# Kernel tuning notes

Hardware: AMD Instinct MI355X
Metric: run time of the kernel (lower is better)

Reference implementation:

```python
import jax, jax.numpy as jnp
import numpy as np

N_NODES = 50000
N_EDGES = 800000
D_IN = 96
D_OUT = 96


def setup_inputs() -> dict:
    key = jax.random.key(0)
    k1, k2, k3, k4, k5 = jax.random.split(key, 5)
    x = jax.random.normal(k1, (N_NODES, D_IN), dtype=jnp.float32)
    edge_w = jax.random.uniform(k2, (N_EDGES,), dtype=jnp.float32)
    weight = jax.random.normal(k3, (D_IN, D_OUT), dtype=jnp.float32) * (1.0 / np.sqrt(D_IN))
    bias = jnp.zeros((D_OUT,), dtype=jnp.float32)
    row = jax.random.randint(k4, (N_EDGES,), 0, N_NODES, dtype=jnp.int32)
    col = jax.random.randint(k5, (N_EDGES,), 0, N_NODES, dtype=jnp.int32)
    return {"x": x, "edge_w": edge_w, "weight": weight, "bias": bias, "row": row, "col": col}


def reference(x, edge_w, weight, bias, row, col):
    # hidden_hat = support @ x, with support given in COO form (row, col, edge_w)
    # gather source-node features, scale by edge weight, scatter-add to destination
    msgs = edge_w[:, None] * x[col]                      # [E, D_in]
    hidden_hat = jax.ops.segment_sum(msgs, row, num_segments=N_NODES)  # [N, D_in]
    # hidden_tilde = hidden_hat @ W + b
    hidden_tilde = jnp.dot(hidden_hat, weight) + bias    # [N, D_out]
    return jax.nn.relu(hidden_tilde)
```

## Files before the change

kernel.cpp:

```cpp
#include <hip/hip_runtime.h>
#include <hip/hip_fp16.h>

#define N_NODES 50000
#define N_EDGES 800000
#define D 96
#define D4 (D / 4)

#define BIN_SH 6
#define BIN_NODES 64
#define NBINS 782
#define MAXB 1536

#define TBLOCKS 782
#define SBLOCKS 196
#define EPB 4082
#define WT_LD 104

typedef _Float16 f16x8 __attribute__((ext_vector_type(8)));
typedef float    f32x4 __attribute__((ext_vector_type(4)));

__global__ __launch_bounds__(256) void transform_scatter(
        const float* __restrict__ x, const float* __restrict__ W,
        const int* __restrict__ row, const int* __restrict__ col,
        const float* __restrict__ edge_w,
        __half* __restrict__ y, int* __restrict__ cursor,
        int2* __restrict__ binned) {
    __shared__ __align__(16) int smem[5000];
    const int t = threadIdx.x;
    const int bid = blockIdx.x;

    if (bid >= TBLOCKS) {
        int* lh    = smem;
        int* gbase = smem + NBINS;
        int* lcur  = smem + 2 * NBINS;
        for (int i = t; i < NBINS; i += 256) { lh[i] = 0; lcur[i] = 0; }
        __syncthreads();
        int e0 = (bid - TBLOCKS) * EPB;
        int e1 = min(e0 + EPB, N_EDGES);
        for (int e = e0 + t; e < e1; e += 256)
            atomicAdd(&lh[row[e] >> BIN_SH], 1);
        __syncthreads();
        for (int i = t; i < NBINS; i += 256)
            gbase[i] = lh[i] ? (i * MAXB + atomicAdd(&cursor[i], lh[i])) : 0;
        __syncthreads();
        for (int e = e0 + t; e < e1; e += 256) {
            int r = row[e];
            int b = r >> BIN_SH;
            int p = atomicAdd(&lcur[b], 1);
            binned[gbase[b] + p] = make_int2(col[e] | ((r & 63) << 16),
                                             __float_as_int(edge_w[e]));
        }
        return;
    }

    _Float16* WT = reinterpret_cast<_Float16*>(smem);
    for (int i = t; i < D * D; i += 256) {
        int k = i / D, n2 = i % D;
        WT[n2 * WT_LD + k] = (_Float16)W[i];
    }
    __syncthreads();

    const int lane = t & 63;
    const int wv   = t >> 6;
    const int wid  = bid * 4 + wv;
    const int n0   = wid * 16;
    if (n0 >= N_NODES) return;

    const int arow = lane & 15;
    const int kgrp = lane >> 4;

    const float4* xr = reinterpret_cast<const float4*>(x) +
                       (long long)(n0 + arow) * D4;
    f16x8 afrag[3];
    #pragma unroll
    for (int ks = 0; ks < 3; ++ks) {
        float4 v0 = xr[ks * 8 + kgrp * 2];
        float4 v1 = xr[ks * 8 + kgrp * 2 + 1];
        f16x8 a;
        a[0] = (_Float16)v0.x; a[1] = (_Float16)v0.y;
        a[2] = (_Float16)v0.z; a[3] = (_Float16)v0.w;
        a[4] = (_Float16)v1.x; a[5] = (_Float16)v1.y;
        a[6] = (_Float16)v1.z; a[7] = (_Float16)v1.w;
        afrag[ks] = a;
    }

    const int bcol = lane & 15;
    #pragma unroll
    for (int nt = 0; nt < 6; ++nt) {
        f32x4 acc = {0.f, 0.f, 0.f, 0.f};
        #pragma unroll
        for (int ks = 0; ks < 3; ++ks) {
            f16x8 b = *reinterpret_cast<const f16x8*>(
                &WT[(nt * 16 + bcol) * WT_LD + ks * 32 + kgrp * 8]);
            acc = __builtin_amdgcn_mfma_f32_16x16x32_f16(afrag[ks], b, acc, 0, 0, 0);
        }
        #pragma unroll
        for (int i = 0; i < 4; ++i) {
            int rrow = kgrp * 4 + i;
            y[(long long)(n0 + rrow) * D + nt * 16 + bcol] = __float2half_rn(acc[i]);
        }
    }
}

__global__ __launch_bounds__(768) void binsort_aggregate(
        const int* __restrict__ cursor, const int2* __restrict__ binned,
        const __half* __restrict__ y, const float* __restrict__ bias,
        float* __restrict__ out) {
    __shared__ int2 recs[MAXB];
    __shared__ int hist[BIN_NODES];
    __shared__ int sc[BIN_NODES];
    __shared__ int lcur[BIN_NODES];
    __shared__ int nodeoff[BIN_NODES + 1];
    int t = threadIdx.x;
    int b = blockIdx.x;
    int base = b * MAXB;
    int size = cursor[b];
    if (size > MAXB) size = MAXB;
    if (t < BIN_NODES) hist[t] = 0;
    __syncthreads();

    int2 rl0, rl1;
    int i0 = t, i1 = t + 768;
    if (i0 < size) { rl0 = binned[base + i0]; atomicAdd(&hist[(rl0.x >> 16) & 63], 1); }
    if (i1 < size) { rl1 = binned[base + i1]; atomicAdd(&hist[(rl1.x >> 16) & 63], 1); }
    __syncthreads();

    int h = 0;
    if (t < BIN_NODES) { h = hist[t]; sc[t] = h; }
    for (int off = 1; off < BIN_NODES; off <<= 1) {
        __syncthreads();
        int a = (t >= off && t < BIN_NODES) ? sc[t - off] : 0;
        __syncthreads();
        if (t < BIN_NODES) sc[t] += a;
    }
    __syncthreads();
    if (t < BIN_NODES) { int excl = sc[t] - h; nodeoff[t] = excl; lcur[t] = excl; }
    if (t == 0) nodeoff[BIN_NODES] = size;
    __syncthreads();

    if (i0 < size) { int lr = (rl0.x >> 16) & 63; int p = atomicAdd(&lcur[lr], 1);
                     recs[p] = make_int2(rl0.x & 0xFFFF, rl0.y); }
    if (i1 < size) { int lr = (rl1.x >> 16) & 63; int p = atomicAdd(&lcur[lr], 1);
                     recs[p] = make_int2(rl1.x & 0xFFFF, rl1.y); }
    __syncthreads();

    const uint4* yu = reinterpret_cast<const uint4*>(y);
    int c = t % 12;
    int g = t / 12;
    int n = (b << BIN_SH) + g;
    if (n >= N_NODES) return;
    int beg = nodeoff[g];
    int end = nodeoff[g + 1];

    float acc[8], acc2[8];
    #pragma unroll
    for (int i = 0; i < 8; ++i) { acc[i] = 0.0f; acc2[i] = 0.0f; }

    int j = beg;
    for (; j + 1 < end; j += 2) {
        int2 r0 = recs[j];
        int2 r1 = recs[j + 1];
        float w0 = __int_as_float(r0.y);
        float w1 = __int_as_float(r1.y);
        uint4 v0 = yu[(long long)r0.x * 12 + c];
        uint4 v1 = yu[(long long)r1.x * 12 + c];
        float2 a0 = __half22float2(*reinterpret_cast<const __half2*>(&v0.x));
        float2 a1 = __half22float2(*reinterpret_cast<const __half2*>(&v0.y));
        float2 a2 = __half22float2(*reinterpret_cast<const __half2*>(&v0.z));
        float2 a3 = __half22float2(*reinterpret_cast<const __half2*>(&v0.w));
        acc[0] = fmaf(w0, a0.x, acc[0]);
        acc[1] = fmaf(w0, a0.y, acc[1]);
        acc[2] = fmaf(w0, a1.x, acc[2]);
        acc[3] = fmaf(w0, a1.y, acc[3]);
        acc[4] = fmaf(w0, a2.x, acc[4]);
        acc[5] = fmaf(w0, a2.y, acc[5]);
        acc[6] = fmaf(w0, a3.x, acc[6]);
        acc[7] = fmaf(w0, a3.y, acc[7]);
        float2 b0 = __half22float2(*reinterpret_cast<const __half2*>(&v1.x));
        float2 b1 = __half22float2(*reinterpret_cast<const __half2*>(&v1.y));
        float2 b2 = __half22float2(*reinterpret_cast<const __half2*>(&v1.z));
        float2 b3 = __half22float2(*reinterpret_cast<const __half2*>(&v1.w));
        acc2[0] = fmaf(w1, b0.x, acc2[0]);
        acc2[1] = fmaf(w1, b0.y, acc2[1]);
        acc2[2] = fmaf(w1, b1.x, acc2[2]);
        acc2[3] = fmaf(w1, b1.y, acc2[3]);
        acc2[4] = fmaf(w1, b2.x, acc2[4]);
        acc2[5] = fmaf(w1, b2.y, acc2[5]);
        acc2[6] = fmaf(w1, b3.x, acc2[6]);
        acc2[7] = fmaf(w1, b3.y, acc2[7]);
    }
    if (j < end) {
        int2 r0 = recs[j];
        float w0 = __int_as_float(r0.y);
        uint4 v0 = yu[(long long)r0.x * 12 + c];
        float2 a0 = __half22float2(*reinterpret_cast<const __half2*>(&v0.x));
        float2 a1 = __half22float2(*reinterpret_cast<const __half2*>(&v0.y));
        float2 a2 = __half22float2(*reinterpret_cast<const __half2*>(&v0.z));
        float2 a3 = __half22float2(*reinterpret_cast<const __half2*>(&v0.w));
        acc[0] = fmaf(w0, a0.x, acc[0]);
        acc[1] = fmaf(w0, a0.y, acc[1]);
        acc[2] = fmaf(w0, a1.x, acc[2]);
        acc[3] = fmaf(w0, a1.y, acc[3]);
        acc[4] = fmaf(w0, a2.x, acc[4]);
        acc[5] = fmaf(w0, a2.y, acc[5]);
        acc[6] = fmaf(w0, a3.x, acc[6]);
        acc[7] = fmaf(w0, a3.y, acc[7]);
    }
    #pragma unroll
    for (int i = 0; i < 8; ++i) acc[i] += acc2[i];

    const float4* b4 = reinterpret_cast<const float4*>(bias);
    float4 ba = b4[c * 2], bb = b4[c * 2 + 1];
    float4 o0, o1;
    o0.x = fmaxf(acc[0] + ba.x, 0.f);
    o0.y = fmaxf(acc[1] + ba.y, 0.f);
    o0.z = fmaxf(acc[2] + ba.z, 0.f);
    o0.w = fmaxf(acc[3] + ba.w, 0.f);
    o1.x = fmaxf(acc[4] + bb.x, 0.f);
    o1.y = fmaxf(acc[5] + bb.y, 0.f);
    o1.z = fmaxf(acc[6] + bb.z, 0.f);
    o1.w = fmaxf(acc[7] + bb.w, 0.f);
    float4* op = reinterpret_cast<float4*>(&out[(long long)n * D + c * 8]);
    op[0] = o0;
    op[1] = o1;
}

__global__ void zero_f32(float* __restrict__ p, long long n) {
    long long i = (long long)blockIdx.x * blockDim.x + threadIdx.x;
    long long stride = (long long)gridDim.x * blockDim.x;
    for (; i < n; i += stride) p[i] = 0.0f;
}

__global__ __launch_bounds__(256) void scatter_edges(
        const float* __restrict__ x, const float* __restrict__ edge_w,
        const int* __restrict__ row, const int* __restrict__ col,
        float* __restrict__ hidden) {
    long long t = (long long)blockIdx.x * blockDim.x + threadIdx.x;
    const long long total = (long long)N_EDGES * D4;
    if (t >= total) return;
    int e = (int)(t / D4);
    int c = (int)(t % D4);
    float w = edge_w[e];
    const float4 v = *reinterpret_cast<const float4*>(&x[(long long)col[e] * D + c * 4]);
    float* o = &hidden[(long long)row[e] * D + c * 4];
    atomicAdd(o + 0, w * v.x);
    atomicAdd(o + 1, w * v.y);
    atomicAdd(o + 2, w * v.z);
    atomicAdd(o + 3, w * v.w);
}

__global__ __launch_bounds__(256) void gemm_bias_relu(
        const float* __restrict__ hidden, const float* __restrict__ W,
        const float* __restrict__ bias, float* __restrict__ out) {
    __shared__ float Ws[D * D];
    __shared__ float bs[D];
    for (int i = threadIdx.x; i < D * D; i += blockDim.x) Ws[i] = W[i];
    if (threadIdx.x < D) bs[threadIdx.x] = bias[threadIdx.x];
    __syncthreads();
    const long long total = (long long)N_NODES * D;
    long long stride = (long long)gridDim.x * blockDim.x;
    for (long long idx = (long long)blockIdx.x * blockDim.x + threadIdx.x;
         idx < total; idx += stride) {
        int n = (int)(idx / D);
        int d = (int)(idx % D);
        const float* hrow = &hidden[(long long)n * D];
        float acc = bs[d];
        #pragma unroll
        for (int k = 0; k < D; ++k) acc = fmaf(hrow[k], Ws[k * D + d], acc);
        out[idx] = fmaxf(acc, 0.0f);
    }
}

extern "C" void kernel_launch(void* const* d_in, const int* in_sizes, int n_in,
                              void* d_out, int out_size, void* d_ws, size_t ws_size,
                              hipStream_t stream) {
    const float* x      = (const float*)d_in[0];
    const float* edge_w = (const float*)d_in[1];
    const float* weight = (const float*)d_in[2];
    const float* bias   = (const float*)d_in[3];
    const int*   row    = (const int*)d_in[4];
    const int*   col    = (const int*)d_in[5];
    float* out = (float*)d_out;

    const size_t yBytes      = (size_t)N_NODES * D * sizeof(__half);
    const size_t binnedBytes = (size_t)NBINS * MAXB * sizeof(int2);
    const size_t curBytes    = (size_t)NBINS * sizeof(int);
    const size_t need = yBytes + binnedBytes + curBytes + 64;

    if (ws_size >= need) {
        char* wsb = (char*)d_ws;
        __half* y      = (__half*)wsb; wsb += yBytes;
        int2*   binned = (int2*)wsb;   wsb += binnedBytes;
        int*    cursor = (int*)wsb;

        hipMemsetAsync(cursor, 0, curBytes, stream);
        transform_scatter<<<TBLOCKS + SBLOCKS, 256, 0, stream>>>(
            x, weight, row, col, edge_w, y, cursor, binned);
        binsort_aggregate<<<NBINS, 768, 0, stream>>>(cursor, binned, y, bias, out);
    } else {
        float* hidden = (float*)d_ws;
        const long long hidden_elems = (long long)N_NODES * D;
        zero_f32<<<2048, 256, 0, stream>>>(hidden, hidden_elems);
        long long total = (long long)N_EDGES * D4;
        scatter_edges<<<(int)((total + 255) / 256), 256, 0, stream>>>(x, edge_w, row,
                                                                      col, hidden);
        gemm_bias_relu<<<2048, 256, 0, stream>>>(hidden, weight, bias, out);
    }
}
```

Baseline: 66.38 us.

## Register-cache edges in scatter pass and sub-sort bin records by source range

The scatter blocks now load each edge's row, col and weight once into registers across two passes instead of rereading them from global memory. The scatter is also split over twice as many blocks with half the edges each. The aggregate kernel sorts records within each destination node by four coarse source-index ranges, so gathers of y rows within a node come in ascending address order, aiming for better L2 and TLB locality. The cost is a 256-entry scan with more barrier steps and a division per record.

Result: faster. 61.84 us (median of 2 runs) (-6.8%).

```diff
diff --git a/kernel.cpp b/kernel.cpp
--- a/kernel.cpp
+++ b/kernel.cpp
@@ -10,10 +10,11 @@
 #define BIN_NODES 64
 #define NBINS 782
 #define MAXB 1536
+#define NB2 256
 
 #define TBLOCKS 782
-#define SBLOCKS 196
-#define EPB 4082
+#define SBLOCKS 392
+#define EPB 2041
 #define WT_LD 104
 
 typedef _Float16 f16x8 __attribute__((ext_vector_type(8)));
@@ -37,18 +38,31 @@
         __syncthreads();
         int e0 = (bid - TBLOCKS) * EPB;
         int e1 = min(e0 + EPB, N_EDGES);
-        for (int e = e0 + t; e < e1; e += 256)
-            atomicAdd(&lh[row[e] >> BIN_SH], 1);
+        int   ex[8];
+        float ew[8];
+        #pragma unroll
+        for (int i = 0; i < 8; ++i) {
+            int e = e0 + t + i * 256;
+            bool v = e < e1;
+            int r  = v ? row[e] : 0;
+            int cc = v ? col[e] : 0;
+            ew[i]  = v ? edge_w[e] : 0.0f;
+            int b  = r >> BIN_SH;
+            ex[i]  = v ? (cc | ((r & 63) << 16) | (b << 22)) : -1;
+            if (v) atomicAdd(&lh[b], 1);
+        }
         __syncthreads();
         for (int i = t; i < NBINS; i += 256)
             gbase[i] = lh[i] ? (i * MAXB + atomicAdd(&cursor[i], lh[i])) : 0;
         __syncthreads();
-        for (int e = e0 + t; e < e1; e += 256) {
-            int r = row[e];
-            int b = r >> BIN_SH;
-            int p = atomicAdd(&lcur[b], 1);
-            binned[gbase[b] + p] = make_int2(col[e] | ((r & 63) << 16),
-                                             __float_as_int(edge_w[e]));
+        #pragma unroll
+        for (int i = 0; i < 8; ++i) {
+            if (ex[i] != -1) {
+                int b = (unsigned)ex[i] >> 22;
+                int p = atomicAdd(&lcur[b], 1);
+                binned[gbase[b] + p] = make_int2(ex[i] & 0x3FFFFF,
+                                                 __float_as_int(ew[i]));
+            }
         }
         return;
     }
@@ -107,41 +121,50 @@
         const __half* __restrict__ y, const float* __restrict__ bias,
         float* __restrict__ out) {
     __shared__ int2 recs[MAXB];
-    __shared__ int hist[BIN_NODES];
-    __shared__ int sc[BIN_NODES];
-    __shared__ int lcur[BIN_NODES];
-    __shared__ int nodeoff[BIN_NODES + 1];
+    __shared__ int hist[NB2];
+    __shared__ int sc[NB2];
+    __shared__ int lcur[NB2];
+    __shared__ int nodeoff[NB2 + 1];
     int t = threadIdx.x;
     int b = blockIdx.x;
     int base = b * MAXB;
     int size = cursor[b];
     if (size > MAXB) size = MAXB;
-    if (t < BIN_NODES) hist[t] = 0;
+    if (t < NB2) hist[t] = 0;
     __syncthreads();
 
     int2 rl0, rl1;
+    int k0 = -1, k1 = -1;
     int i0 = t, i1 = t + 768;
-    if (i0 < size) { rl0 = binned[base + i0]; atomicAdd(&hist[(rl0.x >> 16) & 63], 1); }
-    if (i1 < size) { rl1 = binned[base + i1]; atomicAdd(&hist[(rl1.x >> 16) & 63], 1); }
+    if (i0 < size) {
+        rl0 = binned[base + i0];
+        k0 = (((rl0.x >> 16) & 63) << 2) + (rl0.x & 0xFFFF) / 12500;
+        atomicAdd(&hist[k0], 1);
+    }
+    if (i1 < size) {
+        rl1 = binned[base + i1];
+        k1 = (((rl1.x >> 16) & 63) << 2) + (rl1.x & 0xFFFF) / 12500;
+        atomicAdd(&hist[k1], 1);
+    }
     __syncthreads();
 
     int h = 0;
-    if (t < BIN_NODES) { h = hist[t]; sc[t] = h; }
-    for (int off = 1; off < BIN_NODES; off <<= 1) {
-        __syncthreads();
-        int a = (t >= off && t < BIN_NODES) ? sc[t - off] : 0;
-        __syncthreads();
-        if (t < BIN_NODES) sc[t] += a;
-    }
-    __syncthreads();
-    if (t < BIN_NODES) { int excl = sc[t] - h; nodeoff[t] = excl; lcur[t] = excl; }
-    if (t == 0) nodeoff[BIN_NODES] = size;
-    __syncthreads();
-
-    if (i0 < size) { int lr = (rl0.x >> 16) & 63; int p = atomicAdd(&lcur[lr], 1);
-                     recs[p] = make_int2(rl0.x & 0xFFFF, rl0.y); }
-    if (i1 < size) { int lr = (rl1.x >> 16) & 63; int p = atomicAdd(&lcur[lr], 1);
-                     recs[p] = make_int2(rl1.x & 0xFFFF, rl1.y); }
+    if (t < NB2) { h = hist[t]; sc[t] = h; }
+    for (int off = 1; off < NB2; off <<= 1) {
+        __syncthreads();
+        int a = (t >= off && t < NB2) ? sc[t - off] : 0;
+        __syncthreads();
+        if (t < NB2) sc[t] += a;
+    }
+    __syncthreads();
+    if (t < NB2) { int excl = sc[t] - h; nodeoff[t] = excl; lcur[t] = excl; }
+    if (t == 0) nodeoff[NB2] = size;
+    __syncthreads();
+
+    if (k0 >= 0) { int p = atomicAdd(&lcur[k0], 1);
+                   recs[p] = make_int2(rl0.x & 0xFFFF, rl0.y); }
+    if (k1 >= 0) { int p = atomicAdd(&lcur[k1], 1);
+                   recs[p] = make_int2(rl1.x & 0xFFFF, rl1.y); }
     __syncthreads();
 
     const uint4* yu = reinterpret_cast<const uint4*>(y);
@@ -149,8 +172,8 @@
     int g = t / 12;
     int n = (b << BIN_SH) + g;
     if (n >= N_NODES) return;
-    int beg = nodeoff[g];
-    int end = nodeoff[g + 1];
+    int beg = nodeoff[g << 2];
+    int end = nodeoff[(g + 1) << 2];
 
     float acc[8], acc2[8];
     #pragma unroll
```
